# Kernel tuning notes

Hardware: AMD Instinct MI355X
Metric: run time of the kernel (lower is better)

Reference implementation:

```python
import jax, jax.numpy as jnp
import numpy as np

B, S, D, H = 2, 2048, 1024, 16
DK = D // H

def setup_inputs() -> dict:
    key = jax.random.key(0)
    ks = jax.random.split(key, 12)
    def lin(k):
        kw, kb = jax.random.split(k)
        bound = 1.0 / np.sqrt(D)
        W = jax.random.uniform(kw, (D, D), jnp.float32, -bound, bound)
        b = jax.random.uniform(kb, (D,), jnp.float32, -bound, bound)
        return W, b
    Wq, bq = lin(ks[0]); Wk, bk = lin(ks[1]); Wv, bv = lin(ks[2]); Wo, bo = lin(ks[3])
    q = jax.random.normal(ks[4], (B, S, D), jnp.float32)
    k = jax.random.normal(ks[5], (B, S, D), jnp.float32)
    v = jax.random.normal(ks[6], (B, S, D), jnp.float32)
    mask = jnp.ones((1, 1, S, S), jnp.int32)
    return {"q": q, "k": k, "v": v, "mask": mask,
            "Wq": Wq, "bq": bq, "Wk": Wk, "bk": bk,
            "Wv": Wv, "bv": bv, "Wo": Wo, "bo": bo}

def reference(q, k, v, mask, Wq, bq, Wk, bk, Wv, bv, Wo, bo):
    # torch Linear: y = x @ W.T + b
    Q = (q @ Wq.T + bq).reshape(B, S, H, DK).transpose(0, 2, 1, 3)  # [B,H,S,DK]
    K = (k @ Wk.T + bk).reshape(B, S, H, DK).transpose(0, 2, 1, 3)
    V = (v @ Wv.T + bv).reshape(B, S, H, DK).transpose(0, 2, 1, 3)
    scores = jnp.einsum('bhqd,bhkd->bhqk', Q, K) / jnp.sqrt(jnp.float32(DK))
    scores = jnp.where(mask == 0, jnp.float32(-1e9), scores)
    attn = jax.nn.softmax(scores, axis=-1)
    context = jnp.einsum('bhqk,bhkd->bhqd', attn, V)  # [B,H,S,DK]
    concat = context.transpose(0, 2, 1, 3).reshape(B, S, D)
    return concat @ Wo.T + bo
```

## Files before the change

### kernel.cpp

```cpp
#include <hip/hip_runtime.h>
#include <hip/hip_bf16.h>

#define BB 2
#define SS 2048
#define DD 1024
#define HH 16
#define DKK 64

typedef __hip_bfloat16 bf16;
typedef unsigned short u16;
using frag_ab = __attribute__((ext_vector_type(8))) short;
using frag_cd = __attribute__((ext_vector_type(4))) float;

__device__ inline u16 f2bf(float f) {
    bf16 h = __float2bfloat16(f);
    return *reinterpret_cast<u16*>(&h);
}

__device__ inline void gld16(const void* g, void* l) {
    __builtin_amdgcn_global_load_lds((const __attribute__((address_space(1))) void*)g,
                                     (__attribute__((address_space(3))) void*)l,
                                     16, 0, 0);
}

__device__ inline int swz16(int idx) {
    return idx ^ (((idx >> 6) & 7) << 3);
}

__global__ __launch_bounds__(256) void prep(
    const float* __restrict__ q, const float* __restrict__ k, const float* __restrict__ v,
    const float* __restrict__ Wq, const float* __restrict__ Wk,
    const float* __restrict__ Wv, const float* __restrict__ Wo,
    u16* __restrict__ qb, u16* __restrict__ kb, u16* __restrict__ vb,
    u16* __restrict__ Wqb, u16* __restrict__ Wkb, u16* __restrict__ Wvb, u16* __restrict__ Wob,
    const int* __restrict__ mask, int* __restrict__ flags) {
    int bid = blockIdx.x;
    int t = threadIdx.x;
    if (bid < 8192) {
        const float* src;
        u16* dst;
        int local;
        if (bid < 6144) {
            int ts = bid >> 11;
            local = bid & 2047;
            src = ts == 0 ? q : (ts == 1 ? k : v);
            dst = ts == 0 ? qb : (ts == 1 ? kb : vb);
        } else {
            int wsel = (bid - 6144) >> 9;
            local = (bid - 6144) & 511;
            src = wsel == 0 ? Wq : (wsel == 1 ? Wk : (wsel == 2 ? Wv : Wo));
            dst = wsel == 0 ? Wqb : (wsel == 1 ? Wkb : (wsel == 2 ? Wvb : Wob));
        }
        size_t base = (size_t)local * 2048 + t * 8;
        float4 a = *(const float4*)&src[base];
        float4 b = *(const float4*)&src[base + 4];
        ushort4 u0, u1;
        u0.x = f2bf(a.x); u0.y = f2bf(a.y); u0.z = f2bf(a.z); u0.w = f2bf(a.w);
        u1.x = f2bf(b.x); u1.y = f2bf(b.y); u1.z = f2bf(b.z); u1.w = f2bf(b.w);
        *(ushort4*)&dst[base] = u0;
        *(ushort4*)&dst[base + 4] = u1;
    } else {
        int tile = bid - 8192;
        int qt = tile >> 5, kt = tile & 31;
        __shared__ int f;
        if (t == 0) f = 0;
        __syncthreads();
        int qq = qt * 64 + (t >> 2);
        const int4* row = (const int4*)(mask + (size_t)qq * SS + kt * 64 + (t & 3) * 16);
        int anyz = 0;
#pragma unroll
        for (int i = 0; i < 4; ++i) {
            int4 m4 = row[i];
            anyz |= (m4.x == 0) | (m4.y == 0) | (m4.z == 0) | (m4.w == 0);
        }
        if (anyz) f = 1;
        __syncthreads();
        if (t == 0) flags[tile] = f;
    }
}

__global__ __launch_bounds__(256) void qkv_gemm(
    const u16* __restrict__ Aq, const u16* __restrict__ Ak, const u16* __restrict__ Av,
    const u16* __restrict__ Wq, const u16* __restrict__ Wk, const u16* __restrict__ Wv,
    const float* __restrict__ bq, const float* __restrict__ bk, const float* __restrict__ bv,
    u16* __restrict__ Qo, u16* __restrict__ Ko, u16* __restrict__ Vo) {
    __shared__ u16 As[128 * 32];
    __shared__ u16 Bs[128 * 32];

    int z = blockIdx.z;
    const u16* A = z == 0 ? Aq : (z == 1 ? Ak : Av);
    const u16* W = z == 0 ? Wq : (z == 1 ? Wk : Wv);
    const float* bias = z == 0 ? bq : (z == 1 ? bk : bv);
    u16* out = z == 0 ? Qo : (z == 1 ? Ko : Vo);

    int t = threadIdx.x;
    int m0 = blockIdx.y * 128;
    int n0 = blockIdx.x * 128;
    int w = t >> 6, lane = t & 63;
    int quad = lane >> 4, l16 = lane & 15;
    int wm = w >> 1, wn = w & 1;

    const u16* Ab = A + (size_t)m0 * DD;
    const u16* Wb = W + (size_t)n0 * DD;

    frag_cd acc[4][4];
#pragma unroll
    for (int mt = 0; mt < 4; ++mt)
#pragma unroll
        for (int nt = 0; nt < 4; ++nt) acc[mt][nt] = frag_cd{0.f, 0.f, 0.f, 0.f};

    for (int k0 = 0; k0 < DD; k0 += 32) {
        if (k0) __syncthreads();
#pragma unroll
        for (int i = 0; i < 2; ++i) {
            int c = t + i * 256;
            int row = c >> 2, kc = (c & 3) * 8;
            gld16(Ab + (size_t)row * DD + k0 + kc, &As[c * 8]);
            gld16(Wb + (size_t)row * DD + k0 + kc, &Bs[c * 8]);
        }
        __syncthreads();

        frag_ab af[4], bfr[4];
#pragma unroll
        for (int mt = 0; mt < 4; ++mt)
            af[mt] = *(const frag_ab*)&As[(wm * 64 + mt * 16 + l16) * 32 + quad * 8];
#pragma unroll
        for (int nt = 0; nt < 4; ++nt)
            bfr[nt] = *(const frag_ab*)&Bs[(wn * 64 + nt * 16 + l16) * 32 + quad * 8];
#pragma unroll
        for (int mt = 0; mt < 4; ++mt)
#pragma unroll
            for (int nt = 0; nt < 4; ++nt)
                acc[mt][nt] = __builtin_amdgcn_mfma_f32_16x16x32_bf16(
                    af[mt], bfr[nt], acc[mt][nt], 0, 0, 0);
    }

    float scale = z == 0 ? 0.125f : 1.0f;
#pragma unroll
    for (int nt = 0; nt < 4; ++nt) {
        int n = n0 + wn * 64 + nt * 16 + l16;
        float bv_ = bias[n];
        int h_ = n >> 6, d_ = n & 63;
#pragma unroll
        for (int mt = 0; mt < 4; ++mt) {
            int mb = m0 + wm * 64 + mt * 16 + quad * 4;
            int b_ = mb >> 11, s_ = mb & 2047;
            if (z == 2) {
                ushort4 u;
                u.x = f2bf(acc[mt][nt][0] + bv_);
                u.y = f2bf(acc[mt][nt][1] + bv_);
                u.z = f2bf(acc[mt][nt][2] + bv_);
                u.w = f2bf(acc[mt][nt][3] + bv_);
                *(ushort4*)&out[((size_t)(b_ * HH + h_) * DKK + d_) * SS + s_] = u;
            } else {
#pragma unroll
                for (int r = 0; r < 4; ++r)
                    out[((size_t)(b_ * HH + h_) * SS + s_ + r) * DKK + d_] =
                        f2bf((acc[mt][nt][r] + bv_) * scale);
            }
        }
    }
}

__global__ __launch_bounds__(256) void out_gemm(const u16* __restrict__ A,
                                                const u16* __restrict__ W,
                                                const float* __restrict__ bias,
                                                float* __restrict__ out) {
    __shared__ u16 As[128 * 32];
    __shared__ u16 Bs[128 * 32];

    int t = threadIdx.x;
    int m0 = blockIdx.y * 128;
    int n0 = blockIdx.x * 128;
    int w = t >> 6, lane = t & 63;
    int quad = lane >> 4, l16 = lane & 15;
    int wm = w >> 1, wn = w & 1;

    const u16* Ab = A + (size_t)m0 * DD;
    const u16* Wb = W + (size_t)n0 * DD;

    frag_cd acc[4][4];
#pragma unroll
    for (int mt = 0; mt < 4; ++mt)
#pragma unroll
        for (int nt = 0; nt < 4; ++nt) acc[mt][nt] = frag_cd{0.f, 0.f, 0.f, 0.f};

    for (int k0 = 0; k0 < DD; k0 += 32) {
        if (k0) __syncthreads();
#pragma unroll
        for (int i = 0; i < 2; ++i) {
            int c = t + i * 256;
            int row = c >> 2, kc = (c & 3) * 8;
            gld16(Ab + (size_t)row * DD + k0 + kc, &As[c * 8]);
            gld16(Wb + (size_t)row * DD + k0 + kc, &Bs[c * 8]);
        }
        __syncthreads();

        frag_ab af[4], bfr[4];
#pragma unroll
        for (int mt = 0; mt < 4; ++mt)
            af[mt] = *(const frag_ab*)&As[(wm * 64 + mt * 16 + l16) * 32 + quad * 8];
#pragma unroll
        for (int nt = 0; nt < 4; ++nt)
            bfr[nt] = *(const frag_ab*)&Bs[(wn * 64 + nt * 16 + l16) * 32 + quad * 8];
#pragma unroll
        for (int mt = 0; mt < 4; ++mt)
#pragma unroll
            for (int nt = 0; nt < 4; ++nt)
                acc[mt][nt] = __builtin_amdgcn_mfma_f32_16x16x32_bf16(
                    af[mt], bfr[nt], acc[mt][nt], 0, 0, 0);
    }

#pragma unroll
    for (int nt = 0; nt < 4; ++nt) {
        int n = n0 + wn * 64 + nt * 16 + l16;
        float bv_ = bias[n];
#pragma unroll
        for (int mt = 0; mt < 4; ++mt) {
            int mb = m0 + wm * 64 + mt * 16 + quad * 4;
#pragma unroll
            for (int r = 0; r < 4; ++r)
                out[(size_t)(mb + r) * DD + n] = acc[mt][nt][r] + bv_;
        }
    }
}

__global__ __launch_bounds__(256) void attn_mfma(const u16* __restrict__ Qb,
                                                 const u16* __restrict__ Kb,
                                                 const u16* __restrict__ Vb,
                                                 const int* __restrict__ mask,
                                                 const int* __restrict__ flags,
                                                 u16* __restrict__ C) {
    __shared__ u16 Ks[64 * 64];
    __shared__ u16 Vt[64 * 64];
    __shared__ u16 Pw[4][2][16 * 72];

    int blk = blockIdx.x;
    int Qt = blk & 15;
    int bh = blk >> 4;
    int h = bh & 15;
    int b = bh >> 4;
    int q0 = Qt * 128;

    const u16* Kg = Kb + (size_t)bh * SS * DKK;
    const u16* Vg = Vb + (size_t)bh * DKK * SS;

    int t = threadIdx.x;
    int w = t >> 6;
    int lane = t & 63;
    int quad = lane >> 4;
    int l16 = lane & 15;

    frag_ab bq[2][2];
#pragma unroll
    for (int g = 0; g < 2; ++g) {
        const u16* Qr = Qb + ((size_t)bh * SS + q0 + g * 64 + w * 16 + l16) * DKK;
        bq[g][0] = *(const frag_ab*)&Qr[quad * 8];
        bq[g][1] = *(const frag_ab*)&Qr[32 + quad * 8];
    }

    frag_cd o[2][4];
#pragma unroll
    for (int g = 0; g < 2; ++g)
#pragma unroll
        for (int dt = 0; dt < 4; ++dt) o[g][dt] = frag_cd{0.f, 0.f, 0.f, 0.f};
    float m_prev[2] = {-1e30f, -1e30f};
    float l_run[2] = {0.f, 0.f};

    int vd = t >> 2;
    int vc = (t & 3) * 16;

    int4 kr0, kr1, vr0, vr1;
    {
        const int4* Kt = (const int4*)Kg;
        kr0 = Kt[2 * t]; kr1 = Kt[2 * t + 1];
        const int4* Vr = (const int4*)(Vg + (size_t)vd * SS + vc);
        vr0 = Vr[0]; vr1 = Vr[1];
    }

    for (int kt = 0; kt < 32; ++kt) {
        if (kt) __syncthreads();
        *(int4*)&Ks[swz16(16 * t)] = kr0;
        *(int4*)&Ks[swz16(16 * t + 8)] = kr1;
        *(int4*)&Vt[swz16(vd * 64 + vc)] = vr0;
        *(int4*)&Vt[swz16(vd * 64 + vc + 8)] = vr1;
        if (kt < 31) {
            const int4* Kt = (const int4*)(Kg + (size_t)(kt + 1) * 4096);
            kr0 = Kt[2 * t]; kr1 = Kt[2 * t + 1];
            const int4* Vr = (const int4*)(Vg + (size_t)vd * SS + (kt + 1) * 64 + vc);
            vr0 = Vr[0]; vr1 = Vr[1];
        }
        int az[2];
        az[0] = flags[(Qt * 2) * 32 + kt];
        az[1] = flags[(Qt * 2 + 1) * 32 + kt];
        __syncthreads();

#pragma unroll
        for (int g = 0; g < 2; ++g) {
            float s[4][4];
#pragma unroll
            for (int nt = 0; nt < 4; ++nt) {
                int kr = nt * 16 + l16;
                frag_ab ak0 = *(const frag_ab*)&Ks[swz16(kr * 64 + quad * 8)];
                frag_ab ak1 = *(const frag_ab*)&Ks[swz16(kr * 64 + 32 + quad * 8)];
                frag_cd sf = frag_cd{0.f, 0.f, 0.f, 0.f};
                sf = __builtin_amdgcn_mfma_f32_16x16x32_bf16(ak0, bq[g][0], sf, 0, 0, 0);
                sf = __builtin_amdgcn_mfma_f32_16x16x32_bf16(ak1, bq[g][1], sf, 0, 0, 0);
#pragma unroll
                for (int r = 0; r < 4; ++r) s[nt][r] = sf[r];
            }

            if (az[g]) {
                int qg = q0 + g * 64 + w * 16 + l16;
#pragma unroll
                for (int nt = 0; nt < 4; ++nt)
#pragma unroll
                    for (int r = 0; r < 4; ++r) {
                        int kg = kt * 64 + nt * 16 + quad * 4 + r;
                        if (mask[(size_t)qg * SS + kg] == 0) s[nt][r] = -1e9f;
                    }
            }

            float mc = s[0][0];
#pragma unroll
            for (int nt = 0; nt < 4; ++nt)
#pragma unroll
                for (int r = 0; r < 4; ++r) mc = fmaxf(mc, s[nt][r]);
            mc = fmaxf(mc, __shfl_xor(mc, 16));
            mc = fmaxf(mc, __shfl_xor(mc, 32));
            float mnew = fmaxf(m_prev[g], mc);
            float alpha = __expf(m_prev[g] - mnew);

            float p[4][4];
            float ls = 0.f;
#pragma unroll
            for (int nt = 0; nt < 4; ++nt)
#pragma unroll
                for (int r = 0; r < 4; ++r) {
                    p[nt][r] = __expf(s[nt][r] - mnew);
                    ls += p[nt][r];
                }
            ls += __shfl_xor(ls, 16);
            ls += __shfl_xor(ls, 32);
            l_run[g] = l_run[g] * alpha + ls;
            m_prev[g] = mnew;

#pragma unroll
            for (int dt = 0; dt < 4; ++dt)
#pragma unroll
                for (int r = 0; r < 4; ++r) o[g][dt][r] *= alpha;

#pragma unroll
            for (int nt = 0; nt < 4; ++nt) {
                ushort4 up;
                up.x = f2bf(p[nt][0]); up.y = f2bf(p[nt][1]);
                up.z = f2bf(p[nt][2]); up.w = f2bf(p[nt][3]);
                *(ushort4*)&Pw[w][g][l16 * 72 + nt * 16 + quad * 4] = up;
            }
            frag_ab bp0 = *(const frag_ab*)&Pw[w][g][l16 * 72 + quad * 8];
            frag_ab bp1 = *(const frag_ab*)&Pw[w][g][l16 * 72 + 32 + quad * 8];

#pragma unroll
            for (int dt = 0; dt < 4; ++dt) {
                int dr = dt * 16 + l16;
                frag_ab av0 = *(const frag_ab*)&Vt[swz16(dr * 64 + quad * 8)];
                frag_ab av1 = *(const frag_ab*)&Vt[swz16(dr * 64 + 32 + quad * 8)];
                o[g][dt] = __builtin_amdgcn_mfma_f32_16x16x32_bf16(av0, bp0, o[g][dt], 0, 0, 0);
                o[g][dt] = __builtin_amdgcn_mfma_f32_16x16x32_bf16(av1, bp1, o[g][dt], 0, 0, 0);
            }
        }
    }

#pragma unroll
    for (int g = 0; g < 2; ++g) {
        float inv = 1.f / l_run[g];
        int qg = q0 + g * 64 + w * 16 + l16;
        u16* Crow = C + ((size_t)b * SS + qg) * DD + h * 64;
#pragma unroll
        for (int dt = 0; dt < 4; ++dt) {
            ushort4 u;
            u.x = f2bf(o[g][dt][0] * inv);
            u.y = f2bf(o[g][dt][1] * inv);
            u.z = f2bf(o[g][dt][2] * inv);
            u.w = f2bf(o[g][dt][3] * inv);
            *(ushort4*)&Crow[dt * 16 + quad * 4] = u;
        }
    }
}

extern "C" void kernel_launch(void* const* d_in, const int* in_sizes, int n_in,
                              void* d_out, int out_size, void* d_ws, size_t ws_size,
                              hipStream_t stream) {
    const float* q = (const float*)d_in[0];
    const float* k = (const float*)d_in[1];
    const float* v = (const float*)d_in[2];
    const int* mask = (const int*)d_in[3];
    const float* Wq = (const float*)d_in[4];
    const float* bq = (const float*)d_in[5];
    const float* Wk = (const float*)d_in[6];
    const float* bk = (const float*)d_in[7];
    const float* Wv = (const float*)d_in[8];
    const float* bv = (const float*)d_in[9];
    const float* Wo = (const float*)d_in[10];
    const float* bo = (const float*)d_in[11];
    float* out = (float*)d_out;

    const size_t MB = 1024u * 1024u;
    char* ws = (char*)d_ws;
    u16* qb = (u16*)(ws + 0 * MB);
    u16* kb = (u16*)(ws + 8 * MB);
    u16* vb = (u16*)(ws + 16 * MB);
    u16* Wqb = (u16*)(ws + 24 * MB);
    u16* Wkb = (u16*)(ws + 26 * MB);
    u16* Wvb = (u16*)(ws + 28 * MB);
    u16* Wob = (u16*)(ws + 30 * MB);
    u16* Qb = (u16*)(ws + 32 * MB);
    u16* Kb = (u16*)(ws + 40 * MB);
    u16* Vb = (u16*)(ws + 48 * MB);
    int* flags = (int*)(ws + 56 * MB);
    u16* Cw = qb;

    prep<<<9216, 256, 0, stream>>>(q, k, v, Wq, Wk, Wv, Wo,
                                   qb, kb, vb, Wqb, Wkb, Wvb, Wob, mask, flags);

    dim3 grid(DD / 128, (BB * SS) / 128, 3);
    qkv_gemm<<<grid, 256, 0, stream>>>(qb, kb, vb, Wqb, Wkb, Wvb,
                                       bq, bk, bv, Qb, Kb, Vb);

    attn_mfma<<<BB * HH * (SS / 128), 256, 0, stream>>>(Qb, Kb, Vb, mask, flags, Cw);

    out_gemm<<<dim3(DD / 128, (BB * SS) / 128), 256, 0, stream>>>(Cw, Wob, bo, out);
}
```

Before: 275.7 us.

## Split attention block across eight waves and fold log2e into Q scaling

The attention kernel now launches 512 threads, so each wave owns a single 16-row query group instead of looping over two. Per-thread K/V staging drops to one 16-byte load each, and there is one softmax state per wave. The Q projection scale now includes log2(e), so the softmax uses exp2f instead of __expf. This aims for more waves in flight and less serial work per wave, at the cost of higher register-pressure limits under the new launch bound and more waves contending at each barrier.

```diff
diff --git a/kernel.cpp b/kernel.cpp
--- a/kernel.cpp
+++ b/kernel.cpp
@@ -135,7 +135,7 @@
                     af[mt], bfr[nt], acc[mt][nt], 0, 0, 0);
     }
 
-    float scale = z == 0 ? 0.125f : 1.0f;
+    float scale = z == 0 ? 0.18033688f : 1.0f;
 #pragma unroll
     for (int nt = 0; nt < 4; ++nt) {
         int n = n0 + wn * 64 + nt * 16 + l16;
@@ -225,7 +225,7 @@
     }
 }
 
-__global__ __launch_bounds__(256) void attn_mfma(const u16* __restrict__ Qb,
+__global__ __launch_bounds__(512) void attn_mfma(const u16* __restrict__ Qb,
                                                  const u16* __restrict__ Kb,
                                                  const u16* __restrict__ Vb,
                                                  const int* __restrict__ mask,
@@ -233,7 +233,7 @@
                                                  u16* __restrict__ C) {
     __shared__ u16 Ks[64 * 64];
     __shared__ u16 Vt[64 * 64];
-    __shared__ u16 Pw[4][2][16 * 72];
+    __shared__ u16 Pw[8][16 * 72];
 
     int blk = blockIdx.x;
     int Qt = blk & 15;
@@ -251,138 +251,124 @@
     int quad = lane >> 4;
     int l16 = lane & 15;
 
-    frag_ab bq[2][2];
-#pragma unroll
-    for (int g = 0; g < 2; ++g) {
-        const u16* Qr = Qb + ((size_t)bh * SS + q0 + g * 64 + w * 16 + l16) * DKK;
-        bq[g][0] = *(const frag_ab*)&Qr[quad * 8];
-        bq[g][1] = *(const frag_ab*)&Qr[32 + quad * 8];
-    }
-
-    frag_cd o[2][4];
-#pragma unroll
-    for (int g = 0; g < 2; ++g)
-#pragma unroll
-        for (int dt = 0; dt < 4; ++dt) o[g][dt] = frag_cd{0.f, 0.f, 0.f, 0.f};
-    float m_prev[2] = {-1e30f, -1e30f};
-    float l_run[2] = {0.f, 0.f};
-
-    int vd = t >> 2;
-    int vc = (t & 3) * 16;
-
-    int4 kr0, kr1, vr0, vr1;
+    frag_ab bq0, bq1;
     {
-        const int4* Kt = (const int4*)Kg;
-        kr0 = Kt[2 * t]; kr1 = Kt[2 * t + 1];
-        const int4* Vr = (const int4*)(Vg + (size_t)vd * SS + vc);
-        vr0 = Vr[0]; vr1 = Vr[1];
+        const u16* Qr = Qb + ((size_t)bh * SS + q0 + w * 16 + l16) * DKK;
+        bq0 = *(const frag_ab*)&Qr[quad * 8];
+        bq1 = *(const frag_ab*)&Qr[32 + quad * 8];
+    }
+
+    frag_cd o[4];
+#pragma unroll
+    for (int dt = 0; dt < 4; ++dt) o[dt] = frag_cd{0.f, 0.f, 0.f, 0.f};
+    float m_prev = -1e30f;
+    float l_run = 0.f;
+
+    int vd = t >> 3;
+    int vc = (t & 7) * 8;
+    int fbase = (Qt * 2 + (w >> 2)) * 32;
+
+    int4 kr0, vr0;
+    {
+        kr0 = ((const int4*)Kg)[t];
+        vr0 = *(const int4*)(Vg + (size_t)vd * SS + vc);
     }
 
     for (int kt = 0; kt < 32; ++kt) {
         if (kt) __syncthreads();
-        *(int4*)&Ks[swz16(16 * t)] = kr0;
-        *(int4*)&Ks[swz16(16 * t + 8)] = kr1;
+        *(int4*)&Ks[swz16(8 * t)] = kr0;
         *(int4*)&Vt[swz16(vd * 64 + vc)] = vr0;
-        *(int4*)&Vt[swz16(vd * 64 + vc + 8)] = vr1;
         if (kt < 31) {
-            const int4* Kt = (const int4*)(Kg + (size_t)(kt + 1) * 4096);
-            kr0 = Kt[2 * t]; kr1 = Kt[2 * t + 1];
-            const int4* Vr = (const int4*)(Vg + (size_t)vd * SS + (kt + 1) * 64 + vc);
-            vr0 = Vr[0]; vr1 = Vr[1];
-        }
-        int az[2];
-        az[0] = flags[(Qt * 2) * 32 + kt];
-        az[1] = flags[(Qt * 2 + 1) * 32 + kt];
+            kr0 = ((const int4*)(Kg + (size_t)(kt + 1) * 4096))[t];
+            vr0 = *(const int4*)(Vg + (size_t)vd * SS + (kt + 1) * 64 + vc);
+        }
+        int az = flags[fbase + kt];
         __syncthreads();
 
-#pragma unroll
-        for (int g = 0; g < 2; ++g) {
-            float s[4][4];
-#pragma unroll
-            for (int nt = 0; nt < 4; ++nt) {
-                int kr = nt * 16 + l16;
-                frag_ab ak0 = *(const frag_ab*)&Ks[swz16(kr * 64 + quad * 8)];
-                frag_ab ak1 = *(const frag_ab*)&Ks[swz16(kr * 64 + 32 + quad * 8)];
-                frag_cd sf = frag_cd{0.f, 0.f, 0.f, 0.f};
-                sf = __builtin_amdgcn_mfma_f32_16x16x32_bf16(ak0, bq[g][0], sf, 0, 0, 0);
-                sf = __builtin_amdgcn_mfma_f32_16x16x32_bf16(ak1, bq[g][1], sf, 0, 0, 0);
-#pragma unroll
-                for (int r = 0; r < 4; ++r) s[nt][r] = sf[r];
+        float s[4][4];
+#pragma unroll
+        for (int nt = 0; nt < 4; ++nt) {
+            int kr = nt * 16 + l16;
+            frag_ab ak0 = *(const frag_ab*)&Ks[swz16(kr * 64 + quad * 8)];
+            frag_ab ak1 = *(const frag_ab*)&Ks[swz16(kr * 64 + 32 + quad * 8)];
+            frag_cd sf = frag_cd{0.f, 0.f, 0.f, 0.f};
+            sf = __builtin_amdgcn_mfma_f32_16x16x32_bf16(ak0, bq0, sf, 0, 0, 0);
+            sf = __builtin_amdgcn_mfma_f32_16x16x32_bf16(ak1, bq1, sf, 0, 0, 0);
+#pragma unroll
+            for (int r = 0; r < 4; ++r) s[nt][r] = sf[r];
+        }
+
+        if (az) {
+            int qg = q0 + w * 16 + l16;
+#pragma unroll
+            for (int nt = 0; nt < 4; ++nt)
+#pragma unroll
+                for (int r = 0; r < 4; ++r) {
+                    int kg = kt * 64 + nt * 16 + quad * 4 + r;
+                    if (mask[(size_t)qg * SS + kg] == 0) s[nt][r] = -1e9f;
+                }
+        }
+
+        float mc = s[0][0];
+#pragma unroll
+        for (int nt = 0; nt < 4; ++nt)
+#pragma unroll
+            for (int r = 0; r < 4; ++r) mc = fmaxf(mc, s[nt][r]);
+        mc = fmaxf(mc, __shfl_xor(mc, 16));
+        mc = fmaxf(mc, __shfl_xor(mc, 32));
+        float mnew = fmaxf(m_prev, mc);
+        float alpha = exp2f(m_prev - mnew);
+
+        float p[4][4];
+        float ls = 0.f;
+#pragma unroll
+        for (int nt = 0; nt < 4; ++nt)
+#pragma unroll
+            for (int r = 0; r < 4; ++r) {
+                p[nt][r] = exp2f(s[nt][r] - mnew);
+                ls += p[nt][r];
             }
-
-            if (az[g]) {
-                int qg = q0 + g * 64 + w * 16 + l16;
-#pragma unroll
-                for (int nt = 0; nt < 4; ++nt)
-#pragma unroll
-                    for (int r = 0; r < 4; ++r) {
-                        int kg = kt * 64 + nt * 16 + quad * 4 + r;
-                        if (mask[(size_t)qg * SS + kg] == 0) s[nt][r] = -1e9f;
-                    }
-            }
-
-            float mc = s[0][0];
-#pragma unroll
-            for (int nt = 0; nt < 4; ++nt)
-#pragma unroll
-                for (int r = 0; r < 4; ++r) mc = fmaxf(mc, s[nt][r]);
-            mc = fmaxf(mc, __shfl_xor(mc, 16));
-            mc = fmaxf(mc, __shfl_xor(mc, 32));
-            float mnew = fmaxf(m_prev[g], mc);
-            float alpha = __expf(m_prev[g] - mnew);
-
-            float p[4][4];
-            float ls = 0.f;
-#pragma unroll
-            for (int nt = 0; nt < 4; ++nt)
-#pragma unroll
-                for (int r = 0; r < 4; ++r) {
-                    p[nt][r] = __expf(s[nt][r] - mnew);
-                    ls += p[nt][r];
-                }
-            ls += __shfl_xor(ls, 16);
-            ls += __shfl_xor(ls, 32);
-            l_run[g] = l_run[g] * alpha + ls;
-            m_prev[g] = mnew;
-
-#pragma unroll
-            for (int dt = 0; dt < 4; ++dt)
-#pragma unroll
-                for (int r = 0; r < 4; ++r) o[g][dt][r] *= alpha;
-
-#pragma unroll
-            for (int nt = 0; nt < 4; ++nt) {
-                ushort4 up;
-                up.x = f2bf(p[nt][0]); up.y = f2bf(p[nt][1]);
-                up.z = f2bf(p[nt][2]); up.w = f2bf(p[nt][3]);
-                *(ushort4*)&Pw[w][g][l16 * 72 + nt * 16 + quad * 4] = up;
-            }
-            frag_ab bp0 = *(const frag_ab*)&Pw[w][g][l16 * 72 + quad * 8];
-            frag_ab bp1 = *(const frag_ab*)&Pw[w][g][l16 * 72 + 32 + quad * 8];
-
-#pragma unroll
-            for (int dt = 0; dt < 4; ++dt) {
-                int dr = dt * 16 + l16;
-                frag_ab av0 = *(const frag_ab*)&Vt[swz16(dr * 64 + quad * 8)];
-                frag_ab av1 = *(const frag_ab*)&Vt[swz16(dr * 64 + 32 + quad * 8)];
-                o[g][dt] = __builtin_amdgcn_mfma_f32_16x16x32_bf16(av0, bp0, o[g][dt], 0, 0, 0);
-                o[g][dt] = __builtin_amdgcn_mfma_f32_16x16x32_bf16(av1, bp1, o[g][dt], 0, 0, 0);
-            }
-        }
-    }
-
-#pragma unroll
-    for (int g = 0; g < 2; ++g) {
-        float inv = 1.f / l_run[g];
-        int qg = q0 + g * 64 + w * 16 + l16;
+        ls += __shfl_xor(ls, 16);
+        ls += __shfl_xor(ls, 32);
+        l_run = l_run * alpha + ls;
+        m_prev = mnew;
+
+#pragma unroll
+        for (int dt = 0; dt < 4; ++dt)
+#pragma unroll
+            for (int r = 0; r < 4; ++r) o[dt][r] *= alpha;
+
+#pragma unroll
+        for (int nt = 0; nt < 4; ++nt) {
+            ushort4 up;
+            up.x = f2bf(p[nt][0]); up.y = f2bf(p[nt][1]);
+            up.z = f2bf(p[nt][2]); up.w = f2bf(p[nt][3]);
+            *(ushort4*)&Pw[w][l16 * 72 + nt * 16 + quad * 4] = up;
+        }
+        frag_ab bp0 = *(const frag_ab*)&Pw[w][l16 * 72 + quad * 8];
+        frag_ab bp1 = *(const frag_ab*)&Pw[w][l16 * 72 + 32 + quad * 8];
+
+#pragma unroll
+        for (int dt = 0; dt < 4; ++dt) {
+            int dr = dt * 16 + l16;
+            frag_ab av0 = *(const frag_ab*)&Vt[swz16(dr * 64 + quad * 8)];
+            frag_ab av1 = *(const frag_ab*)&Vt[swz16(dr * 64 + 32 + quad * 8)];
+            o[dt] = __builtin_amdgcn_mfma_f32_16x16x32_bf16(av0, bp0, o[dt], 0, 0, 0);
+            o[dt] = __builtin_amdgcn_mfma_f32_16x16x32_bf16(av1, bp1, o[dt], 0, 0, 0);
+        }
+    }
+
+    {
+        float inv = 1.f / l_run;
+        int qg = q0 + w * 16 + l16;
         u16* Crow = C + ((size_t)b * SS + qg) * DD + h * 64;
 #pragma unroll
         for (int dt = 0; dt < 4; ++dt) {
             ushort4 u;
-            u.x = f2bf(o[g][dt][0] * inv);
-            u.y = f2bf(o[g][dt][1] * inv);
-            u.z = f2bf(o[g][dt][2] * inv);
-            u.w = f2bf(o[g][dt][3] * inv);
+            u.x = f2bf(o[dt][0] * inv);
+            u.y = f2bf(o[dt][1] * inv);
+            u.z = f2bf(o[dt][2] * inv);
+            u.w = f2bf(o[dt][3] * inv);
             *(ushort4*)&Crow[dt * 16 + quad * 4] = u;
         }
     }
@@ -427,7 +413,7 @@
     qkv_gemm<<<grid, 256, 0, stream>>>(qb, kb, vb, Wqb, Wkb, Wvb,
                                        bq, bk, bv, Qb, Kb, Vb);
 
-    attn_mfma<<<BB * HH * (SS / 128), 256, 0, stream>>>(Qb, Kb, Vb, mask, flags, Cw);
+    attn_mfma<<<BB * HH * (SS / 128), 512, 0, stream>>>(Qb, Kb, Vb, mask, flags, Cw);
 
     out_gemm<<<dim3(DD / 128, (BB * SS) / 128), 256, 0, stream>>>(Cw, Wob, bo, out);
 }
```

Result: faster. 263.4 us (-4.4%).
